# Optimization experiments

Measured on AMD Instinct MI355X. Metric: run time of the kernel, lower is better.

## Reference

```python
import jax, jax.numpy as jnp
import numpy as np

T, C, H, N = 1024, 2048, 32, 64
D_LORA, D_G = 64, 128

def _ln(x, w, b, eps=1e-5):
    m = x.mean(-1, keepdims=True)
    v = ((x - m) ** 2).mean(-1, keepdims=True)
    return (x - m) * jax.lax.rsqrt(v + eps) * w + b

def setup_inputs():
    key = jax.random.key(0)
    ks = iter(jax.random.split(key, 48))
    rn = lambda shape, s=1.0: jax.random.normal(next(ks), shape, dtype=jnp.float32) * s
    return {
        "x": rn((T, C)),
        "x_prev_att": rn((C,)),
        "vk_state": rn((H, N, N), 0.1),
        "x_prev_ffn": rn((C,)),
        "v_first": rn((T, C)),
        "ln1_w": jnp.ones((C,), jnp.float32), "ln1_b": jnp.zeros((C,), jnp.float32),
        "x_r": rn((C,), 0.1), "x_w": rn((C,), 0.1), "x_k": rn((C,), 0.1),
        "x_v": rn((C,), 0.1), "x_a": rn((C,), 0.1), "x_g": rn((C,), 0.1),
        "w0": rn((C,), 0.1), "w1": rn((C, D_LORA), 0.02), "w2": rn((D_LORA, C), 0.02),
        "a0": rn((C,), 0.1), "a1": rn((C, D_LORA), 0.02), "a2": rn((D_LORA, C), 0.02),
        "v0": rn((C,), 0.1), "v1": rn((C, D_LORA), 0.02), "v2": rn((D_LORA, C), 0.02),
        "g1": rn((C, D_G), 0.02), "g2": rn((D_G, C), 0.02),
        "k_k": rn((C,), 0.1), "k_a": rn((C,), 0.1), "r_k": rn((C,), 0.1),
        "R_": rn((C, C), 0.02), "K_": rn((C, C), 0.02),
        "V_": rn((C, C), 0.02), "O_": rn((C, C), 0.02),
        "lnx_w": jnp.ones((C,), jnp.float32), "lnx_b": jnp.zeros((C,), jnp.float32),
        "ln2_w": jnp.ones((C,), jnp.float32), "ln2_b": jnp.zeros((C,), jnp.float32),
        "ffn_x_k": rn((C,), 0.1),
        "ffn_K": rn((C, 4 * C), 0.02), "ffn_V": rn((4 * C, C), 0.02),
    }

def reference(x, x_prev_att, vk_state, x_prev_ffn, v_first, ln1_w, ln1_b,
              x_r, x_w, x_k, x_v, x_a, x_g, w0, w1, w2, a0, a1, a2,
              v0, v1, v2, g1, g2, k_k, k_a, r_k, R_, K_, V_, O_,
              lnx_w, lnx_b, ln2_w, ln2_b, ffn_x_k, ffn_K, ffn_V):
    # ---- TMix: RWKV-7 time mixing (layer_id = 1, so v_first blend is active) ----
    xln = _ln(x, ln1_w, ln1_b)                                  # [T, C]
    dx = jnp.concatenate([x_prev_att[None, :], xln[:-1]], axis=0) - xln  # token shift
    xr, xw, xk, xv, xa, xg = (xln + dx * m for m in (x_r, x_w, x_k, x_v, x_a, x_g))
    r = xr @ R_
    w = jnp.tanh(xw @ w1) @ w2
    k = xk @ K_
    v = xv @ V_
    a = jax.nn.sigmoid(a0 + (xa @ a1) @ a2)
    g = jax.nn.sigmoid(xg @ g1) @ g2
    kk = (k * k_k).reshape(T, H, N)
    kk = kk / jnp.maximum(jnp.linalg.norm(kk, axis=-1, keepdims=True), 1e-12)  # L2 normalize per head
    k = k * (1.0 + (a - 1.0) * k_a)
    v = v + (v_first - v) * jax.nn.sigmoid(v0 + (xv @ v1) @ v2)  # layer_id != 0 path
    w = jnp.exp(-0.606531 * jax.nn.sigmoid(w0 + w))               # per-channel decay in (0,1)
    rh, kh, vh = r.reshape(T, H, N), k.reshape(T, H, N), v.reshape(T, H, N)
    ah, wh = a.reshape(T, H, N), w.reshape(T, H, N)

    def step(state, inp):
        # state: [H, N, N]; generalized delta rule: state*w + state@(-kk)(kk*a)^T + v k^T
        w_t, kk_t, a_t, k_t, v_t, r_t = inp
        ab = jnp.einsum('hi,hj->hij', -kk_t, kk_t * a_t)
        vk = jnp.einsum('hi,hj->hij', v_t, k_t)
        state = state * w_t[:, None, :] + jnp.einsum('hij,hjk->hik', state, ab) + vk
        return state, jnp.einsum('hij,hj->hi', state, r_t)

    vk_state, outs = jax.lax.scan(step, vk_state, (wh, kk, ah, kh, vh, rh))  # outs: [T, H, N]
    # group norm over H groups, eps = 0.00064, affine per-channel
    m = outs.mean(-1, keepdims=True)
    var = ((outs - m) ** 2).mean(-1, keepdims=True)
    gn = ((outs - m) * jax.lax.rsqrt(var + 0.00064)).reshape(T, C) * lnx_w + lnx_b
    bonus = ((r * k * r_k).reshape(T, H, N).sum(-1, keepdims=True) * vh).reshape(T, C)
    x = x + ((gn + bonus) * g) @ O_
    # ---- CMix: gated squared-ReLU MLP ----
    xln2 = _ln(x, ln2_w, ln2_b)
    dx2 = jnp.concatenate([x_prev_ffn[None, :], xln2[:-1]], axis=0) - xln2
    kf = jax.nn.relu((xln2 + dx2 * ffn_x_k) @ ffn_K) ** 2
    x = x + kf @ ffn_V
    return x
```

## Files before the change

### kernel.cpp

```cpp
#include <hip/hip_runtime.h>
#include <hip/hip_bf16.h>


#define T_ 1024
#define C_ 2048
#define H_ 32
#define NH 64

typedef __attribute__((ext_vector_type(8))) short short8v;
typedef __attribute__((ext_vector_type(4))) float f32x4;

__device__ __forceinline__ float bf2f(unsigned short u) {
  union { float f; unsigned int i; } c; c.i = ((unsigned int)u) << 16; return c.f;
}
__device__ __forceinline__ unsigned short f2bf(float f) {
  union { float f; unsigned int i; } c; c.f = f;
  unsigned int x = c.i;
  return (unsigned short)((x + 0x7fffu + ((x >> 16) & 1u)) >> 16);
}
__device__ __forceinline__ float sigm(float x) { return 1.f / (1.f + __expf(-x)); }

__device__ __forceinline__ void load8bf(const unsigned short* p, float* o) {
  union { int4 v; unsigned short u[8]; } c;
  c.v = *(const int4*)p;
#pragma unroll
  for (int i = 0; i < 8; ++i) o[i] = bf2f(c.u[i]);
}
__device__ __forceinline__ void store8bf(unsigned short* p, const float* o) {
  union { int4 v; unsigned short u[8]; } c;
#pragma unroll
  for (int i = 0; i < 8; ++i) c.u[i] = f2bf(o[i]);
  *(int4*)p = c.v;
}
__device__ __forceinline__ void load8f(const float* p, float* o) {
  float4 a = ((const float4*)p)[0], b = ((const float4*)p)[1];
  o[0] = a.x; o[1] = a.y; o[2] = a.z; o[3] = a.w;
  o[4] = b.x; o[5] = b.y; o[6] = b.z; o[7] = b.w;
}
__device__ __forceinline__ void load4f(const float* p, float* o) {
  float4 a = *(const float4*)p;
  o[0] = a.x; o[1] = a.y; o[2] = a.z; o[3] = a.w;
}

#define GLD16(g, l)                                                        \
  __builtin_amdgcn_global_load_lds(                                        \
      (const __attribute__((address_space(1))) void*)(g),                  \
      (__attribute__((address_space(3))) void*)(l), 16, 0, 0)

__global__ __launch_bounds__(256) void lnmix6_kernel(
    const float* __restrict__ x, const float* __restrict__ xprev,
    const float* __restrict__ lw, const float* __restrict__ lb,
    const float* __restrict__ mr, const float* __restrict__ mw,
    const float* __restrict__ mk, const float* __restrict__ mv,
    const float* __restrict__ ma, const float* __restrict__ mg,
    unsigned short* xr, unsigned short* xw, unsigned short* xk,
    unsigned short* xv, unsigned short* xa, unsigned short* xg) {
  int t = blockIdx.x, tid = threadIdx.x, c = tid * 8;
  float cur[8], prv[8];
  load8f(x + (size_t)t * C_ + c, cur);
  if (t == 0) load8f(xprev + c, prv);
  else load8f(x + (size_t)(t - 1) * C_ + c, prv);
  float sc = 0.f, qc = 0.f, sp = 0.f, qp = 0.f;
#pragma unroll
  for (int i = 0; i < 8; ++i) {
    sc += cur[i]; qc += cur[i] * cur[i];
    sp += prv[i]; qp += prv[i] * prv[i];
  }
  for (int m = 1; m < 64; m <<= 1) {
    sc += __shfl_xor(sc, m); qc += __shfl_xor(qc, m);
    sp += __shfl_xor(sp, m); qp += __shfl_xor(qp, m);
  }
  __shared__ float r4[4][4];
  if ((tid & 63) == 0) {
    r4[tid >> 6][0] = sc; r4[tid >> 6][1] = qc;
    r4[tid >> 6][2] = sp; r4[tid >> 6][3] = qp;
  }
  __syncthreads();
  sc = r4[0][0] + r4[1][0] + r4[2][0] + r4[3][0];
  qc = r4[0][1] + r4[1][1] + r4[2][1] + r4[3][1];
  sp = r4[0][2] + r4[1][2] + r4[2][2] + r4[3][2];
  qp = r4[0][3] + r4[1][3] + r4[2][3] + r4[3][3];
  float mc = sc * (1.f / C_);
  float rc = rsqrtf(qc * (1.f / C_) - mc * mc + 1e-5f);
  float mp = sp * (1.f / C_);
  float rp = rsqrtf(qp * (1.f / C_) - mp * mp + 1e-5f);
  float cw[8], cb[8];
  load8f(lw + c, cw); load8f(lb + c, cb);
  float curn[8], prvn[8];
#pragma unroll
  for (int i = 0; i < 8; ++i) {
    curn[i] = (cur[i] - mc) * rc * cw[i] + cb[i];
    prvn[i] = (t == 0) ? prv[i] : (prv[i] - mp) * rp * cw[i] + cb[i];
  }
  float cf[8], o[8];
  const float* coefs[6] = {mr, mw, mk, mv, ma, mg};
  unsigned short* outs6[6] = {xr, xw, xk, xv, xa, xg};
#pragma unroll
  for (int a = 0; a < 6; ++a) {
    load8f(coefs[a] + c, cf);
#pragma unroll
    for (int i = 0; i < 8; ++i) o[i] = curn[i] + (prvn[i] - curn[i]) * cf[i];
    store8bf(outs6[a] + (size_t)t * C_ + c, o);
  }
}

__global__ __launch_bounds__(256) void lnmix1_kernel(
    const float* __restrict__ x, const float* __restrict__ xprev,
    const float* __restrict__ lw, const float* __restrict__ lb,
    const float* __restrict__ coef, unsigned short* __restrict__ out) {
  int t = blockIdx.x, tid = threadIdx.x, c = tid * 8;
  float cur[8], prv[8];
  load8f(x + (size_t)t * C_ + c, cur);
  if (t == 0) load8f(xprev + c, prv);
  else load8f(x + (size_t)(t - 1) * C_ + c, prv);
  float sc = 0.f, qc = 0.f, sp = 0.f, qp = 0.f;
#pragma unroll
  for (int i = 0; i < 8; ++i) {
    sc += cur[i]; qc += cur[i] * cur[i];
    sp += prv[i]; qp += prv[i] * prv[i];
  }
  for (int m = 1; m < 64; m <<= 1) {
    sc += __shfl_xor(sc, m); qc += __shfl_xor(qc, m);
    sp += __shfl_xor(sp, m); qp += __shfl_xor(qp, m);
  }
  __shared__ float r4[4][4];
  if ((tid & 63) == 0) {
    r4[tid >> 6][0] = sc; r4[tid >> 6][1] = qc;
    r4[tid >> 6][2] = sp; r4[tid >> 6][3] = qp;
  }
  __syncthreads();
  sc = r4[0][0] + r4[1][0] + r4[2][0] + r4[3][0];
  qc = r4[0][1] + r4[1][1] + r4[2][1] + r4[3][1];
  sp = r4[0][2] + r4[1][2] + r4[2][2] + r4[3][2];
  qp = r4[0][3] + r4[1][3] + r4[2][3] + r4[3][3];
  float mc = sc * (1.f / C_);
  float rc = rsqrtf(qc * (1.f / C_) - mc * mc + 1e-5f);
  float mp = sp * (1.f / C_);
  float rp = rsqrtf(qp * (1.f / C_) - mp * mp + 1e-5f);
  float cw[8], cb[8], cf[8], o[8];
  load8f(lw + c, cw); load8f(lb + c, cb); load8f(coef + c, cf);
#pragma unroll
  for (int i = 0; i < 8; ++i) {
    float cn = (cur[i] - mc) * rc * cw[i] + cb[i];
    float pn = (t == 0) ? prv[i] : (prv[i] - mp) * rp * cw[i] + cb[i];
    o[i] = cn + (pn - cn) * cf[i];
  }
  store8bf(out + (size_t)t * C_ + c, o);
}

__device__ __forceinline__ void transpose_tile(
    const float* __restrict__ in, unsigned short* __restrict__ out,
    int R, int Cc, int bx, int by, unsigned short (*tile)[80]) {
  int c0 = bx * 64, r0 = by * 64;
  int rr = threadIdx.x >> 4, cq = threadIdx.x & 15;
#pragma unroll
  for (int i = 0; i < 4; ++i) {
    int r = rr + i * 16;
    float4 v = *(const float4*)(in + (size_t)(r0 + r) * Cc + c0 + cq * 4);
    tile[cq * 4 + 0][r] = f2bf(v.x);
    tile[cq * 4 + 1][r] = f2bf(v.y);
    tile[cq * 4 + 2][r] = f2bf(v.z);
    tile[cq * 4 + 3][r] = f2bf(v.w);
  }
  __syncthreads();
  int cr = threadIdx.x >> 2, rg = threadIdx.x & 3;
  int4 w0 = *(const int4*)&tile[cr][rg * 16];
  int4 w1 = *(const int4*)&tile[cr][rg * 16 + 8];
  unsigned short* op = out + (size_t)(c0 + cr) * R + r0 + rg * 16;
  *(int4*)op = w0;
  *(int4*)(op + 8) = w1;
}

__global__ __launch_bounds__(256) void transpose_kernel(
    const float* in0, const float* in1, const float* in2,
    unsigned short* o0, unsigned short* o1, unsigned short* o2,
    int R, int Cc) {
  const float* in = blockIdx.z == 0 ? in0 : (blockIdx.z == 1 ? in1 : in2);
  unsigned short* out = blockIdx.z == 0 ? o0 : (blockIdx.z == 1 ? o1 : o2);
  __shared__ __align__(16) unsigned short tile[64][80];
  transpose_tile(in, out, R, Cc, blockIdx.x, blockIdx.y, tile);
}

template <int EPI>
__global__ __launch_bounds__(256) void gemm2_kernel(
    const unsigned short* A0, const unsigned short* A1, const unsigned short* A2,
    const unsigned short* B0, const unsigned short* B1, const unsigned short* B2,
    void* C0, void* C1, void* C2, const float* __restrict__ addsrc,
    int M, int K, int N) {
  int z = blockIdx.z;
  const unsigned short* A = z == 0 ? A0 : (z == 1 ? A1 : A2);
  const unsigned short* Bt = z == 0 ? B0 : (z == 1 ? B1 : B2);
  void* Cout = z == 0 ? C0 : (z == 1 ? C1 : C2);
  __shared__ __align__(16) unsigned short As[2][128 * 32];
  __shared__ __align__(16) unsigned short Bs[2][128 * 32];
  const int tid = threadIdx.x, lane = tid & 63, wid = tid >> 6;
  const int bm = blockIdx.y * 128, bn = blockIdx.x * 128;
  const int wr = wid >> 1, wc = wid & 1;
  const int mrow = lane & 15, krow = lane >> 4;
  auto stage = [&](int buf, int kt) {
#pragma unroll
    for (int q = 0; q < 2; ++q) {
      int s = q * 2048 + tid * 8;
      int m = s >> 5, k = s & 31;
      GLD16(A + (size_t)(bm + m) * K + kt + k, &As[buf][s]);
      GLD16(Bt + (size_t)(bn + m) * K + kt + k, &Bs[buf][s]);
    }
  };
  f32x4 acc[4][4] = {};
  stage(0, 0);
  __syncthreads();
  int buf = 0;
  for (int kt = 0; kt < K; kt += 32) {
    if (kt + 32 < K) stage(buf ^ 1, kt + 32);
    short8v af[4], bfrag[4];
#pragma unroll
    for (int i = 0; i < 4; ++i)
      af[i] = *(const short8v*)&As[buf][(wr * 64 + i * 16 + mrow) * 32 + krow * 8];
#pragma unroll
    for (int j = 0; j < 4; ++j)
      bfrag[j] = *(const short8v*)&Bs[buf][(wc * 64 + j * 16 + mrow) * 32 + krow * 8];
#pragma unroll
    for (int i = 0; i < 4; ++i)
#pragma unroll
      for (int j = 0; j < 4; ++j)
        acc[i][j] = __builtin_amdgcn_mfma_f32_16x16x32_bf16(af[i], bfrag[j], acc[i][j], 0, 0, 0);
    __syncthreads();
    buf ^= 1;
  }
#pragma unroll
  for (int i = 0; i < 4; ++i)
#pragma unroll
    for (int j = 0; j < 4; ++j)
#pragma unroll
      for (int e = 0; e < 4; ++e) {
        int grow = bm + wr * 64 + i * 16 + (lane >> 4) * 4 + e;
        int gcol = bn + wc * 64 + j * 16 + (lane & 15);
        size_t off = (size_t)grow * N + gcol;
        float v = acc[i][j][e];
        if constexpr (EPI == 0) ((float*)Cout)[off] = v;
        else if constexpr (EPI == 1) ((float*)Cout)[off] = addsrc[off] + v;
        else { float r = v > 0.f ? v : 0.f; ((unsigned short*)Cout)[off] = f2bf(r * r); }
      }
}

__global__ __launch_bounds__(256) void gemm2ks_kernel(
    const unsigned short* __restrict__ A, const unsigned short* __restrict__ Bt,
    unsigned short* __restrict__ P, int M, int KH, int Ktot, int N) {
  int kz = blockIdx.z;
  const size_t kbase = (size_t)kz * KH;
  __shared__ __align__(16) unsigned short As[2][128 * 32];
  __shared__ __align__(16) unsigned short Bs[2][128 * 32];
  const int tid = threadIdx.x, lane = tid & 63, wid = tid >> 6;
  const int bm = blockIdx.y * 128, bn = blockIdx.x * 128;
  const int wr = wid >> 1, wc = wid & 1;
  const int mrow = lane & 15, krow = lane >> 4;
  auto stage = [&](int buf, int kt) {
#pragma unroll
    for (int q = 0; q < 2; ++q) {
      int s = q * 2048 + tid * 8;
      int m = s >> 5, k = s & 31;
      GLD16(A + (size_t)(bm + m) * Ktot + kbase + kt + k, &As[buf][s]);
      GLD16(Bt + (size_t)(bn + m) * Ktot + kbase + kt + k, &Bs[buf][s]);
    }
  };
  f32x4 acc[4][4] = {};
  stage(0, 0);
  __syncthreads();
  int buf = 0;
  for (int kt = 0; kt < KH; kt += 32) {
    if (kt + 32 < KH) stage(buf ^ 1, kt + 32);
    short8v af[4], bfrag[4];
#pragma unroll
    for (int i = 0; i < 4; ++i)
      af[i] = *(const short8v*)&As[buf][(wr * 64 + i * 16 + mrow) * 32 + krow * 8];
#pragma unroll
    for (int j = 0; j < 4; ++j)
      bfrag[j] = *(const short8v*)&Bs[buf][(wc * 64 + j * 16 + mrow) * 32 + krow * 8];
#pragma unroll
    for (int i = 0; i < 4; ++i)
#pragma unroll
      for (int j = 0; j < 4; ++j)
        acc[i][j] = __builtin_amdgcn_mfma_f32_16x16x32_bf16(af[i], bfrag[j], acc[i][j], 0, 0, 0);
    __syncthreads();
    buf ^= 1;
  }
  unsigned short* Pz = P + (size_t)kz * M * N;
#pragma unroll
  for (int i = 0; i < 4; ++i)
#pragma unroll
    for (int j = 0; j < 4; ++j)
#pragma unroll
      for (int e = 0; e < 4; ++e) {
        int grow = bm + wr * 64 + i * 16 + (lane >> 4) * 4 + e;
        int gcol = bn + wc * 64 + j * 16 + (lane & 15);
        Pz[(size_t)grow * N + gcol] = f2bf(acc[i][j][e]);
      }
}

__global__ __launch_bounds__(256) void gemm2ks3_kernel(
    const unsigned short* A0, const unsigned short* A1, const unsigned short* A2,
    const unsigned short* B0, const unsigned short* B1, const unsigned short* B2,
    unsigned short* __restrict__ P, int M, int KH, int Ktot, int N) {
  int z = blockIdx.z;
  int batch = z % 3, kz = z / 3;
  const unsigned short* A = batch == 0 ? A0 : (batch == 1 ? A1 : A2);
  const unsigned short* Bt = batch == 0 ? B0 : (batch == 1 ? B1 : B2);
  const size_t kbase = (size_t)kz * KH;
  __shared__ __align__(16) unsigned short As[2][128 * 32];
  __shared__ __align__(16) unsigned short Bs[2][128 * 32];
  const int tid = threadIdx.x, lane = tid & 63, wid = tid >> 6;
  const int bm = blockIdx.y * 128, bn = blockIdx.x * 128;
  const int wr = wid >> 1, wc = wid & 1;
  const int mrow = lane & 15, krow = lane >> 4;
  auto stage = [&](int buf, int kt) {
#pragma unroll
    for (int q = 0; q < 2; ++q) {
      int s = q * 2048 + tid * 8;
      int m = s >> 5, k = s & 31;
      GLD16(A + (size_t)(bm + m) * Ktot + kbase + kt + k, &As[buf][s]);
      GLD16(Bt + (size_t)(bn + m) * Ktot + kbase + kt + k, &Bs[buf][s]);
    }
  };
  f32x4 acc[4][4] = {};
  stage(0, 0);
  __syncthreads();
  int buf = 0;
  for (int kt = 0; kt < KH; kt += 32) {
    if (kt + 32 < KH) stage(buf ^ 1, kt + 32);
    short8v af[4], bfrag[4];
#pragma unroll
    for (int i = 0; i < 4; ++i)
      af[i] = *(const short8v*)&As[buf][(wr * 64 + i * 16 + mrow) * 32 + krow * 8];
#pragma unroll
    for (int j = 0; j < 4; ++j)
      bfrag[j] = *(const short8v*)&Bs[buf][(wc * 64 + j * 16 + mrow) * 32 + krow * 8];
#pragma unroll
    for (int i = 0; i < 4; ++i)
#pragma unroll
      for (int j = 0; j < 4; ++j)
        acc[i][j] = __builtin_amdgcn_mfma_f32_16x16x32_bf16(af[i], bfrag[j], acc[i][j], 0, 0, 0);
    __syncthreads();
    buf ^= 1;
  }
  unsigned short* Pz = P + (size_t)z * M * N;
#pragma unroll
  for (int i = 0; i < 4; ++i)
#pragma unroll
    for (int j = 0; j < 4; ++j)
#pragma unroll
      for (int e = 0; e < 4; ++e) {
        int grow = bm + wr * 64 + i * 16 + (lane >> 4) * 4 + e;
        int gcol = bn + wc * 64 + j * 16 + (lane & 15);
        Pz[(size_t)grow * N + gcol] = f2bf(acc[i][j][e]);
      }
}

__global__ __launch_bounds__(256) void add5_kernel(
    const float* __restrict__ a, const unsigned short* __restrict__ p,
    float* __restrict__ o) {
  size_t i = ((size_t)blockIdx.x * 256 + threadIdx.x) * 8;
  const size_t TC = (size_t)T_ * C_;
  float va[8], v0[8], v1[8], v2[8], v3[8], r[8];
  load8f(a + i, va);
  load8bf(p + i, v0);
  load8bf(p + i + TC, v1);
  load8bf(p + i + 2 * TC, v2);
  load8bf(p + i + 3 * TC, v3);
#pragma unroll
  for (int k = 0; k < 8; ++k) r[k] = va[k] + v0[k] + v1[k] + v2[k] + v3[k];
  *(float4*)(o + i) = make_float4(r[0], r[1], r[2], r[3]);
  *(float4*)(o + i + 4) = make_float4(r[4], r[5], r[6], r[7]);
}

__global__ __launch_bounds__(256) void add5tr_kernel(
    const float* __restrict__ a, const unsigned short* __restrict__ p,
    float* __restrict__ o, const float* __restrict__ fK,
    unsigned short* __restrict__ fKt) {
  int bid = blockIdx.x;
  if (bid < 1024) {
    size_t i = ((size_t)bid * 256 + threadIdx.x) * 8;
    const size_t TC = (size_t)T_ * C_;
    float va[8], v0[8], v1[8], v2[8], v3[8], r[8];
    load8f(a + i, va);
    load8bf(p + i, v0);
    load8bf(p + i + TC, v1);
    load8bf(p + i + 2 * TC, v2);
    load8bf(p + i + 3 * TC, v3);
#pragma unroll
    for (int k = 0; k < 8; ++k) r[k] = va[k] + v0[k] + v1[k] + v2[k] + v3[k];
    *(float4*)(o + i) = make_float4(r[0], r[1], r[2], r[3]);
    *(float4*)(o + i + 4) = make_float4(r[4], r[5], r[6], r[7]);
    return;
  }
  __shared__ __align__(16) unsigned short tile[64][80];
  int idx = bid - 1024;
  transpose_tile(fK, fKt, C_, 4 * C_, idx & 127, idx >> 7, tile);
}

__global__ __launch_bounds__(256) void gemm_ks3_kernel(
    const unsigned short* A0, const unsigned short* A1, const unsigned short* A2,
    const unsigned short* B0, const unsigned short* B1, const unsigned short* B2,
    float* P0, float* P1, float* P2, int K, int N) {
  int mz = blockIdx.z >> 3, kz = blockIdx.z & 7;
  const unsigned short* A = mz == 0 ? A0 : (mz == 1 ? A1 : A2);
  const unsigned short* Bt = mz == 0 ? B0 : (mz == 1 ? B1 : B2);
  float* partial = mz == 0 ? P0 : (mz == 1 ? P1 : P2);
  __shared__ __align__(16) unsigned short As[2][128 * 32];
  __shared__ __align__(16) unsigned short Bs[2][64 * 32];
  const int tid = threadIdx.x, lane = tid & 63, wid = tid >> 6;
  const int bn = blockIdx.x * 64, bm = blockIdx.y * 128;
  const int wr = wid >> 1, wc = wid & 1;
  const int mrow = lane & 15, krow = lane >> 4;
  auto stage = [&](int buf, int kt) {
#pragma unroll
    for (int q = 0; q < 2; ++q) {
      int s = q * 2048 + tid * 8;
      int m = s >> 5, k = s & 31;
      GLD16(A + (size_t)(bm + m) * K + kt + k, &As[buf][s]);
    }
    {
      int s = tid * 8;
      int n = s >> 5, k = s & 31;
      GLD16(Bt + (size_t)(bn + n) * K + kt + k, &Bs[buf][s]);
    }
  };
  f32x4 acc[4][2] = {};
  int k0 = kz * 256;
  stage(0, k0);
  __syncthreads();
  int buf = 0;
  for (int kt = k0; kt < k0 + 256; kt += 32) {
    if (kt + 32 < k0 + 256) stage(buf ^ 1, kt + 32);
    short8v af[4], bfrag[2];
#pragma unroll
    for (int i = 0; i < 4; ++i)
      af[i] = *(const short8v*)&As[buf][(wr * 64 + i * 16 + mrow) * 32 + krow * 8];
#pragma unroll
    for (int j = 0; j < 2; ++j)
      bfrag[j] = *(const short8v*)&Bs[buf][(wc * 32 + j * 16 + mrow) * 32 + krow * 8];
#pragma unroll
    for (int i = 0; i < 4; ++i)
#pragma unroll
      for (int j = 0; j < 2; ++j)
        acc[i][j] = __builtin_amdgcn_mfma_f32_16x16x32_bf16(af[i], bfrag[j], acc[i][j], 0, 0, 0);
    __syncthreads();
    buf ^= 1;
  }
#pragma unroll
  for (int i = 0; i < 4; ++i)
#pragma unroll
    for (int j = 0; j < 2; ++j)
#pragma unroll
      for (int e = 0; e < 4; ++e) {
        int row = bm + wr * 64 + i * 16 + (lane >> 4) * 4 + e;
        int col = bn + wc * 32 + j * 16 + (lane & 15);
        partial[((size_t)kz * 1024 + row) * N + col] = acc[i][j][e];
      }
}

__global__ __launch_bounds__(256) void gemm_ks_kernel(
    const unsigned short* __restrict__ A, const unsigned short* __restrict__ Bt,
    float* __restrict__ partial, int K, int N) {
  __shared__ __align__(16) unsigned short As[2][128 * 32];
  __shared__ __align__(16) unsigned short Bs[2][64 * 32];
  const int tid = threadIdx.x, lane = tid & 63, wid = tid >> 6;
  const int bn = blockIdx.x * 64, bm = blockIdx.y * 128, kz = blockIdx.z;
  const int wr = wid >> 1, wc = wid & 1;
  const int mrow = lane & 15, krow = lane >> 4;
  auto stage = [&](int buf, int kt) {
#pragma unroll
    for (int q = 0; q < 2; ++q) {
      int s = q * 2048 + tid * 8;
      int m = s >> 5, k = s & 31;
      GLD16(A + (size_t)(bm + m) * K + kt + k, &As[buf][s]);
    }
    {
      int s = tid * 8;
      int n = s >> 5, k = s & 31;
      GLD16(Bt + (size_t)(bn + n) * K + kt + k, &Bs[buf][s]);
    }
  };
  f32x4 acc[4][2] = {};
  int k0 = kz * 256;
  stage(0, k0);
  __syncthreads();
  int buf = 0;
  for (int kt = k0; kt < k0 + 256; kt += 32) {
    if (kt + 32 < k0 + 256) stage(buf ^ 1, kt + 32);
    short8v af[4], bfrag[2];
#pragma unroll
    for (int i = 0; i < 4; ++i)
      af[i] = *(const short8v*)&As[buf][(wr * 64 + i * 16 + mrow) * 32 + krow * 8];
#pragma unroll
    for (int j = 0; j < 2; ++j)
      bfrag[j] = *(const short8v*)&Bs[buf][(wc * 32 + j * 16 + mrow) * 32 + krow * 8];
#pragma unroll
    for (int i = 0; i < 4; ++i)
#pragma unroll
      for (int j = 0; j < 2; ++j)
        acc[i][j] = __builtin_amdgcn_mfma_f32_16x16x32_bf16(af[i], bfrag[j], acc[i][j], 0, 0, 0);
    __syncthreads();
    buf ^= 1;
  }
#pragma unroll
  for (int i = 0; i < 4; ++i)
#pragma unroll
    for (int j = 0; j < 2; ++j)
#pragma unroll
      for (int e = 0; e < 4; ++e) {
        int row = bm + wr * 64 + i * 16 + (lane >> 4) * 4 + e;
        int col = bn + wc * 32 + j * 16 + (lane & 15);
        partial[((size_t)kz * 1024 + row) * N + col] = acc[i][j][e];
      }
}

__global__ __launch_bounds__(128) void lora_combine_kernel(
    const float* __restrict__ pw, const float* __restrict__ pa,
    const float* __restrict__ pv, const float* __restrict__ pg,
    unsigned short* __restrict__ hw, unsigned short* __restrict__ ha,
    unsigned short* __restrict__ hv, unsigned short* __restrict__ hg) {
  int t = blockIdx.x, which = blockIdx.y, tid = threadIdx.x;
  int Nl = (which == 3) ? 128 : 64;
  if (tid >= Nl) return;
  const float* p = which == 0 ? pw : which == 1 ? pa : which == 2 ? pv : pg;
  float s = 0.f;
#pragma unroll
  for (int kz = 0; kz < 8; ++kz) s += p[((size_t)kz * 1024 + t) * Nl + tid];
  float r = which == 0 ? tanhf(s) : (which == 3 ? sigm(s) : s);
  unsigned short* o = which == 0 ? hw : which == 1 ? ha : which == 2 ? hv : hg;
  o[t * Nl + tid] = f2bf(r);
}

__global__ __launch_bounds__(256) void post_kernel(
    const unsigned short* __restrict__ qRKV, const float* __restrict__ wpre,
    const float* __restrict__ apre, const float* __restrict__ vpre,
    const float* __restrict__ vfirst, const float* __restrict__ w0,
    const float* __restrict__ a0, const float* __restrict__ v0_,
    const float* __restrict__ k_k, const float* __restrict__ k_a,
    float* __restrict__ scanin) {
  int t = blockIdx.x, tid = threadIdx.x;
  int c = tid * 8, h = tid >> 3, j = c & 63;
  size_t o = (size_t)t * C_ + c;
  const size_t TC = (size_t)T_ * C_;
  float rv[8], kv[8], vv[8], t0[8], wv[8], av[8], vp[8], vf[8];
  load8bf(qRKV + o, rv);          load8bf(qRKV + 3 * TC + o, t0);
#pragma unroll
  for (int i = 0; i < 8; ++i) rv[i] += t0[i];
  load8bf(qRKV + TC + o, kv);     load8bf(qRKV + 4 * TC + o, t0);
#pragma unroll
  for (int i = 0; i < 8; ++i) kv[i] += t0[i];
  load8bf(qRKV + 2 * TC + o, vv); load8bf(qRKV + 5 * TC + o, t0);
#pragma unroll
  for (int i = 0; i < 8; ++i) vv[i] += t0[i];
  load8f(wpre + o, wv); load8f(apre + o, av); load8f(vpre + o, vp);
  load8f(vfirst + o, vf);
  float ckk[8], cka[8], cw0[8], ca0[8], cv0[8];
  load8f(k_k + c, ckk); load8f(k_a + c, cka); load8f(w0 + c, cw0);
  load8f(a0 + c, ca0); load8f(v0_ + c, cv0);
  float kk[8]; float ss = 0.f;
#pragma unroll
  for (int i = 0; i < 8; ++i) { kk[i] = kv[i] * ckk[i]; ss += kk[i] * kk[i]; }
  ss += __shfl_xor(ss, 1); ss += __shfl_xor(ss, 2); ss += __shfl_xor(ss, 4);
  float rdn = 1.f / fmaxf(sqrtf(ss), 1e-12f);
  float sw[8], skn[8], scc[8], sk2[8], sv[8];
#pragma unroll
  for (int i = 0; i < 8; ++i) {
// ... 153 lines not shown
  const float* x       = (const float*)d_in[0];
  const float* xprev_a = (const float*)d_in[1];
  const float* vk0     = (const float*)d_in[2];
  const float* xprev_f = (const float*)d_in[3];
  const float* vfirst  = (const float*)d_in[4];
  const float* ln1w = (const float*)d_in[5];
  const float* ln1b = (const float*)d_in[6];
  const float* m_r = (const float*)d_in[7];
  const float* m_w = (const float*)d_in[8];
  const float* m_k = (const float*)d_in[9];
  const float* m_v = (const float*)d_in[10];
  const float* m_a = (const float*)d_in[11];
  const float* m_g = (const float*)d_in[12];
  const float* w0 = (const float*)d_in[13];
  const float* w1 = (const float*)d_in[14];
  const float* w2 = (const float*)d_in[15];
  const float* a0 = (const float*)d_in[16];
  const float* a1 = (const float*)d_in[17];
  const float* a2 = (const float*)d_in[18];
  const float* v0 = (const float*)d_in[19];
  const float* v1 = (const float*)d_in[20];
  const float* v2 = (const float*)d_in[21];
  const float* g1 = (const float*)d_in[22];
  const float* g2 = (const float*)d_in[23];
  const float* k_k = (const float*)d_in[24];
  const float* k_a = (const float*)d_in[25];
  const float* r_k = (const float*)d_in[26];
  const float* R_ = (const float*)d_in[27];
  const float* K_ = (const float*)d_in[28];
  const float* V_ = (const float*)d_in[29];
  const float* O_ = (const float*)d_in[30];
  const float* lnxw = (const float*)d_in[31];
  const float* lnxb = (const float*)d_in[32];
  const float* ln2w = (const float*)d_in[33];
  const float* ln2b = (const float*)d_in[34];
  const float* fxk = (const float*)d_in[35];
  const float* fK = (const float*)d_in[36];
  const float* fV = (const float*)d_in[37];
  float* out = (float*)d_out;

  char* ws = (char*)d_ws;
  const size_t MB = 1ull << 20;
  unsigned short* attin = (unsigned short*)(ws + 0 * MB);
  unsigned short* xr    = (unsigned short*)(ws + 4 * MB);
  unsigned short* xw    = (unsigned short*)(ws + 8 * MB);
  unsigned short* xk    = (unsigned short*)(ws + 12 * MB);
  unsigned short* xv    = (unsigned short*)(ws + 16 * MB);
  unsigned short* xa    = (unsigned short*)(ws + 20 * MB);
  unsigned short* xg    = (unsigned short*)(ws + 24 * MB);
  float* wpre  = (float*)(ws + 4 * MB);
  float* apre  = (float*)(ws + 12 * MB);
  float* vpre  = (float*)(ws + 20 * MB);
  unsigned short* fVt = (unsigned short*)(ws + 4 * MB);
  unsigned short* xkf = (unsigned short*)(ws + 36 * MB);
  unsigned short* qRKV = (unsigned short*)(ws + 28 * MB);
  float* outsb = (float*)(ws + 52 * MB);
  unsigned short* Ot = (unsigned short*)(ws + 60 * MB);
  float* x_att = (float*)(ws + 60 * MB);
  float* g_buf = (float*)(ws + 76 * MB);
  float* scanin = (float*)(ws + 84 * MB);
  unsigned short* Rt  = (unsigned short*)(ws + 84 * MB);
  unsigned short* Kt  = (unsigned short*)(ws + 92 * MB);
  unsigned short* Vt  = (unsigned short*)(ws + 100 * MB);
  unsigned short* qO  = (unsigned short*)(ws + 84 * MB);
  unsigned short* hffn = (unsigned short*)(ws + 84 * MB);
  unsigned short* fKt  = (unsigned short*)(ws + 100 * MB);
  unsigned short* pF   = (unsigned short*)(ws + 100 * MB);
  unsigned short* w1t = (unsigned short*)(ws + 0);
  unsigned short* a1t = (unsigned short*)(ws + 262144);
  unsigned short* v1t = (unsigned short*)(ws + 524288);
  unsigned short* g1t = (unsigned short*)(ws + 786432);
  unsigned short* w2t = (unsigned short*)(ws + 0);
  unsigned short* a2t = (unsigned short*)(ws + 262144);
  unsigned short* v2t = (unsigned short*)(ws + 524288);
  unsigned short* g2t = (unsigned short*)(ws + 786432);
  unsigned short* hwb = (unsigned short*)(ws + 1376256);
  unsigned short* hab = (unsigned short*)(ws + 1507328);
  unsigned short* hvb = (unsigned short*)(ws + 1638400);
  unsigned short* hgb = (unsigned short*)(ws + 1769472);
  float* pw = (float*)(ws + 2 * MB);
  float* pa = (float*)(ws + 4 * MB);
  float* pv = (float*)(ws + 6 * MB);
  float* pg = (float*)(ws + 8 * MB);

  lnmix6_kernel<<<T_, 256, 0, stream>>>(x, xprev_a, ln1w, ln1b,
                                        m_r, m_w, m_k, m_v, m_a, m_g,
                                        xr, xw, xk, xv, xa, xg);
  transpose_kernel<<<dim3(32, 32, 3), 256, 0, stream>>>(R_, K_, V_, Rt, Kt, Vt, C_, C_);
  gemm2ks3_kernel<<<dim3(16, 8, 6), 256, 0, stream>>>(xr, xk, xv, Rt, Kt, Vt,
                                                      qRKV, T_, 1024, C_, C_);
  transpose_kernel<<<dim3(1, 32, 3), 256, 0, stream>>>(w1, a1, v1, w1t, a1t, v1t, C_, 64);
  transpose_kernel<<<dim3(2, 32, 1), 256, 0, stream>>>(g1, g1, g1, g1t, g1t, g1t, C_, 128);
  gemm_ks3_kernel<<<dim3(1, 8, 24), 256, 0, stream>>>(xw, xa, xv, w1t, a1t, v1t,
                                                      pw, pa, pv, C_, 64);
  gemm_ks_kernel<<<dim3(2, 8, 8), 256, 0, stream>>>(xg, g1t, pg, C_, 128);
  lora_combine_kernel<<<dim3(T_, 4), 128, 0, stream>>>(pw, pa, pv, pg, hwb, hab, hvb, hgb);
  transpose_kernel<<<dim3(32, 1, 3), 256, 0, stream>>>(w2, a2, v2, w2t, a2t, v2t, 64, C_);
  transpose_kernel<<<dim3(32, 2, 1), 256, 0, stream>>>(g2, g2, g2, g2t, g2t, g2t, 128, C_);
  gemm2_kernel<0><<<dim3(16, 8, 3), 256, 0, stream>>>(hwb, hab, hvb, w2t, a2t, v2t,
                                                      wpre, apre, vpre, nullptr, T_, 64, C_);
  gemm2_kernel<0><<<dim3(16, 8, 1), 256, 0, stream>>>(hgb, hgb, hgb, g2t, g2t, g2t,
                                                      g_buf, g_buf, g_buf, nullptr, T_, 128, C_);
  post_kernel<<<T_, 256, 0, stream>>>(qRKV, wpre, apre, vpre, vfirst,
                                      w0, a0, v0, k_k, k_a, scanin);
  scanfuse_kernel<<<5632, 256, 0, stream>>>(scanin, vk0, outsb, O_, Ot, fV, fVt);
  gnb_kernel<<<T_, 256, 0, stream>>>(outsb, scanin, g_buf, r_k, lnxw, lnxb, attin);
  gemm2ks_kernel<<<dim3(16, 8, 4), 256, 0, stream>>>(attin, Ot, qO, T_, 512, C_, C_);
  add5tr_kernel<<<5120, 256, 0, stream>>>(x, qO, x_att, fK, fKt);
  lnmix1_kernel<<<T_, 256, 0, stream>>>(x_att, xprev_f, ln2w, ln2b, fxk, xkf);
  gemm2_kernel<2><<<dim3(64, 8, 1), 256, 0, stream>>>(xkf, xkf, xkf, fKt, fKt, fKt,
                                                      hffn, hffn, hffn, nullptr, T_, C_, 4 * C_);
  gemm2ks_kernel<<<dim3(16, 8, 4), 256, 0, stream>>>(hffn, fVt, pF, T_, 2048, 4 * C_, C_);
  add5_kernel<<<1024, 256, 0, stream>>>(x_att, pF, out);
}
```

Measured before the change: 451.2 us.

## Merge LN-mix with all weight transposes and batch the front GEMMs into one launch

Folds the six weight transposes into the first layer-norm/mix kernel as extra blocks. It also merges the R/K/V split-K GEMM and the LoRA down-projection GEMMs into a single heterogeneous launch, and the four LoRA up-projection GEMMs into one launch. This cuts around nine kernel launches and lets small LoRA GEMMs fill the GPU alongside the large ones, at the cost of relocating workspace buffers so the merged stages do not alias. Blocks in the fused kernels take divergent paths and share one LDS allocation sized for the largest role.

```diff
diff --git a/kernel.cpp b/kernel.cpp
--- a/kernel.cpp
+++ b/kernel.cpp
@@ -47,15 +47,78 @@
       (const __attribute__((address_space(1))) void*)(g),                  \
       (__attribute__((address_space(3))) void*)(l), 16, 0, 0)
 
-__global__ __launch_bounds__(256) void lnmix6_kernel(
+__device__ __forceinline__ void transpose_tile(
+    const float* __restrict__ in, unsigned short* __restrict__ out,
+    int R, int Cc, int bx, int by, unsigned short (*tile)[80]) {
+  int c0 = bx * 64, r0 = by * 64;
+  int rr = threadIdx.x >> 4, cq = threadIdx.x & 15;
+#pragma unroll
+  for (int i = 0; i < 4; ++i) {
+    int r = rr + i * 16;
+    float4 v = *(const float4*)(in + (size_t)(r0 + r) * Cc + c0 + cq * 4);
+    tile[cq * 4 + 0][r] = f2bf(v.x);
+    tile[cq * 4 + 1][r] = f2bf(v.y);
+    tile[cq * 4 + 2][r] = f2bf(v.z);
+    tile[cq * 4 + 3][r] = f2bf(v.w);
+  }
+  __syncthreads();
+  int cr = threadIdx.x >> 2, rg = threadIdx.x & 3;
+  int4 w0 = *(const int4*)&tile[cr][rg * 16];
+  int4 w1 = *(const int4*)&tile[cr][rg * 16 + 8];
+  unsigned short* op = out + (size_t)(c0 + cr) * R + r0 + rg * 16;
+  *(int4*)op = w0;
+  *(int4*)(op + 8) = w1;
+}
+
+__global__ __launch_bounds__(256) void lnmix6tr_kernel(
     const float* __restrict__ x, const float* __restrict__ xprev,
     const float* __restrict__ lw, const float* __restrict__ lb,
     const float* __restrict__ mr, const float* __restrict__ mw,
     const float* __restrict__ mk, const float* __restrict__ mv,
     const float* __restrict__ ma, const float* __restrict__ mg,
     unsigned short* xr, unsigned short* xw, unsigned short* xk,
-    unsigned short* xv, unsigned short* xa, unsigned short* xg) {
-  int t = blockIdx.x, tid = threadIdx.x, c = tid * 8;
+    unsigned short* xv, unsigned short* xa, unsigned short* xg,
+    const float* R_, const float* K_, const float* V_,
+    unsigned short* Rt, unsigned short* Kt, unsigned short* Vt,
+    const float* w1, const float* a1, const float* v1,
+    unsigned short* w1t, unsigned short* a1t, unsigned short* v1t,
+    const float* g1, unsigned short* g1t,
+    const float* w2, const float* a2, const float* v2,
+    unsigned short* w2t, unsigned short* a2t, unsigned short* v2t,
+    const float* g2, unsigned short* g2t) {
+  __shared__ __align__(16) unsigned short tile[64][80];
+  __shared__ float r4[4][4];
+  int bid = blockIdx.x;
+  if (bid >= 1024) {
+    int idx = bid - 1024;
+    if (idx < 3072) {
+      const float* in = idx < 1024 ? R_ : (idx < 2048 ? K_ : V_);
+      unsigned short* out = idx < 1024 ? Rt : (idx < 2048 ? Kt : Vt);
+      int r = idx & 1023;
+      transpose_tile(in, out, C_, C_, r & 31, r >> 5, tile);
+      return;
+    }
+    idx -= 3072;
+    if (idx < 96) {
+      const float* in = idx < 32 ? w1 : (idx < 64 ? a1 : v1);
+      unsigned short* out = idx < 32 ? w1t : (idx < 64 ? a1t : v1t);
+      transpose_tile(in, out, C_, 64, 0, idx & 31, tile);
+      return;
+    }
+    idx -= 96;
+    if (idx < 64) { transpose_tile(g1, g1t, C_, 128, idx & 1, idx >> 1, tile); return; }
+    idx -= 64;
+    if (idx < 96) {
+      const float* in = idx < 32 ? w2 : (idx < 64 ? a2 : v2);
+      unsigned short* out = idx < 32 ? w2t : (idx < 64 ? a2t : v2t);
+      transpose_tile(in, out, 64, C_, idx & 31, 0, tile);
+      return;
+    }
+    idx -= 96;
+    transpose_tile(g2, g2t, 128, C_, idx & 31, idx >> 5, tile);
+    return;
+  }
+  int t = bid, tid = threadIdx.x, c = tid * 8;
   float cur[8], prv[8];
   load8f(x + (size_t)t * C_ + c, cur);
   if (t == 0) load8f(xprev + c, prv);
@@ -70,7 +133,6 @@
     sc += __shfl_xor(sc, m); qc += __shfl_xor(qc, m);
     sp += __shfl_xor(sp, m); qp += __shfl_xor(qp, m);
   }
-  __shared__ float r4[4][4];
   if ((tid & 63) == 0) {
     r4[tid >> 6][0] = sc; r4[tid >> 6][1] = qc;
     r4[tid >> 6][2] = sp; r4[tid >> 6][3] = qp;
@@ -146,39 +208,6 @@
     o[i] = cn + (pn - cn) * cf[i];
   }
   store8bf(out + (size_t)t * C_ + c, o);
-}
-
-__device__ __forceinline__ void transpose_tile(
-    const float* __restrict__ in, unsigned short* __restrict__ out,
-    int R, int Cc, int bx, int by, unsigned short (*tile)[80]) {
-  int c0 = bx * 64, r0 = by * 64;
-  int rr = threadIdx.x >> 4, cq = threadIdx.x & 15;
-#pragma unroll
-  for (int i = 0; i < 4; ++i) {
-    int r = rr + i * 16;
-    float4 v = *(const float4*)(in + (size_t)(r0 + r) * Cc + c0 + cq * 4);
-    tile[cq * 4 + 0][r] = f2bf(v.x);
-    tile[cq * 4 + 1][r] = f2bf(v.y);
-    tile[cq * 4 + 2][r] = f2bf(v.z);
-    tile[cq * 4 + 3][r] = f2bf(v.w);
-  }
-  __syncthreads();
-  int cr = threadIdx.x >> 2, rg = threadIdx.x & 3;
-  int4 w0 = *(const int4*)&tile[cr][rg * 16];
-  int4 w1 = *(const int4*)&tile[cr][rg * 16 + 8];
-  unsigned short* op = out + (size_t)(c0 + cr) * R + r0 + rg * 16;
-  *(int4*)op = w0;
-  *(int4*)(op + 8) = w1;
-}
-
-__global__ __launch_bounds__(256) void transpose_kernel(
-    const float* in0, const float* in1, const float* in2,
-    unsigned short* o0, unsigned short* o1, unsigned short* o2,
-    int R, int Cc) {
-  const float* in = blockIdx.z == 0 ? in0 : (blockIdx.z == 1 ? in1 : in2);
-  unsigned short* out = blockIdx.z == 0 ? o0 : (blockIdx.z == 1 ? o1 : o2);
-  __shared__ __align__(16) unsigned short tile[64][80];
-  transpose_tile(in, out, R, Cc, blockIdx.x, blockIdx.y, tile);
 }
 
 template <int EPI>
@@ -243,6 +272,66 @@
       }
 }
 
+__global__ __launch_bounds__(256) void gemm2up_kernel(
+    const unsigned short* hwb, const unsigned short* hab,
+    const unsigned short* hvb, const unsigned short* hgb,
+    const unsigned short* w2t, const unsigned short* a2t,
+    const unsigned short* v2t, const unsigned short* g2t,
+    float* wpre, float* apre, float* vpre, float* g_buf) {
+  int z = blockIdx.z;
+  const unsigned short* A = z == 0 ? hwb : (z == 1 ? hab : (z == 2 ? hvb : hgb));
+  const unsigned short* Bt = z == 0 ? w2t : (z == 1 ? a2t : (z == 2 ? v2t : g2t));
+  float* Cout = z == 0 ? wpre : (z == 1 ? apre : (z == 2 ? vpre : g_buf));
+  const int K = (z == 3) ? 128 : 64;
+  const int N = C_;
+  __shared__ __align__(16) unsigned short As[2][128 * 32];
+  __shared__ __align__(16) unsigned short Bs[2][128 * 32];
+  const int tid = threadIdx.x, lane = tid & 63, wid = tid >> 6;
+  const int bm = blockIdx.y * 128, bn = blockIdx.x * 128;
+  const int wr = wid >> 1, wc = wid & 1;
+  const int mrow = lane & 15, krow = lane >> 4;
+  auto stage = [&](int buf, int kt) {
+#pragma unroll
+    for (int q = 0; q < 2; ++q) {
+      int s = q * 2048 + tid * 8;
+      int m = s >> 5, k = s & 31;
+      GLD16(A + (size_t)(bm + m) * K + kt + k, &As[buf][s]);
+      GLD16(Bt + (size_t)(bn + m) * K + kt + k, &Bs[buf][s]);
+    }
+  };
+  f32x4 acc[4][4] = {};
+  stage(0, 0);
+  __syncthreads();
+  int buf = 0;
+  for (int kt = 0; kt < K; kt += 32) {
+    if (kt + 32 < K) stage(buf ^ 1, kt + 32);
+    short8v af[4], bfrag[4];
+#pragma unroll
+    for (int i = 0; i < 4; ++i)
+      af[i] = *(const short8v*)&As[buf][(wr * 64 + i * 16 + mrow) * 32 + krow * 8];
+#pragma unroll
+    for (int j = 0; j < 4; ++j)
+      bfrag[j] = *(const short8v*)&Bs[buf][(wc * 64 + j * 16 + mrow) * 32 + krow * 8];
+#pragma unroll
+    for (int i = 0; i < 4; ++i)
+#pragma unroll
+      for (int j = 0; j < 4; ++j)
+        acc[i][j] = __builtin_amdgcn_mfma_f32_16x16x32_bf16(af[i], bfrag[j], acc[i][j], 0, 0, 0);
+    __syncthreads();
+    buf ^= 1;
+  }
+#pragma unroll
+  for (int i = 0; i < 4; ++i)
+#pragma unroll
+    for (int j = 0; j < 4; ++j)
+#pragma unroll
+      for (int e = 0; e < 4; ++e) {
+        int grow = bm + wr * 64 + i * 16 + (lane >> 4) * 4 + e;
+        int gcol = bn + wc * 64 + j * 16 + (lane & 15);
+        Cout[(size_t)grow * N + gcol] = acc[i][j][e];
+      }
+}
+
 __global__ __launch_bounds__(256) void gemm2ks_kernel(
     const unsigned short* __restrict__ A, const unsigned short* __restrict__ Bt,
     unsigned short* __restrict__ P, int M, int KH, int Ktot, int N) {
@@ -297,61 +386,136 @@
       }
 }
 
-__global__ __launch_bounds__(256) void gemm2ks3_kernel(
-    const unsigned short* A0, const unsigned short* A1, const unsigned short* A2,
-    const unsigned short* B0, const unsigned short* B1, const unsigned short* B2,
-    unsigned short* __restrict__ P, int M, int KH, int Ktot, int N) {
-  int z = blockIdx.z;
-  int batch = z % 3, kz = z / 3;
-  const unsigned short* A = batch == 0 ? A0 : (batch == 1 ? A1 : A2);
-  const unsigned short* Bt = batch == 0 ? B0 : (batch == 1 ? B1 : B2);
-  const size_t kbase = (size_t)kz * KH;
-  __shared__ __align__(16) unsigned short As[2][128 * 32];
-  __shared__ __align__(16) unsigned short Bs[2][128 * 32];
+__global__ __launch_bounds__(256) void bigemm_kernel(
+    const unsigned short* xr, const unsigned short* xk, const unsigned short* xv,
+    const unsigned short* Rt, const unsigned short* Kt, const unsigned short* Vt,
+    unsigned short* __restrict__ qRKV,
+    const unsigned short* xw, const unsigned short* xa, const unsigned short* xg,
+    const unsigned short* w1t, const unsigned short* a1t, const unsigned short* v1t,
+    const unsigned short* g1t,
+    float* pw, float* pa, float* pv, float* pg) {
+  __shared__ __align__(16) unsigned short smem[16384];
+  const int bid = blockIdx.x;
   const int tid = threadIdx.x, lane = tid & 63, wid = tid >> 6;
-  const int bm = blockIdx.y * 128, bn = blockIdx.x * 128;
   const int wr = wid >> 1, wc = wid & 1;
   const int mrow = lane & 15, krow = lane >> 4;
+  unsigned short* As0 = smem;
+  if (bid < 768) {
+    int bz = bid >> 7, rem = bid & 127;
+    int bx = rem & 15, by = rem >> 4;
+    int batch = bz % 3, kz = bz / 3;
+    const unsigned short* A = batch == 0 ? xr : (batch == 1 ? xk : xv);
+    const unsigned short* Bt = batch == 0 ? Rt : (batch == 1 ? Kt : Vt);
+    unsigned short* Bs0 = smem + 8192;
+    const size_t kbase = (size_t)kz * 1024;
+    const int bm = by * 128, bn = bx * 128;
+    auto stage = [&](int buf, int kt) {
+#pragma unroll
+      for (int q = 0; q < 2; ++q) {
+        int s = q * 2048 + tid * 8;
+        int m = s >> 5, k = s & 31;
+        GLD16(A + (size_t)(bm + m) * C_ + kbase + kt + k, &As0[buf * 4096 + s]);
+        GLD16(Bt + (size_t)(bn + m) * C_ + kbase + kt + k, &Bs0[buf * 4096 + s]);
+      }
+    };
+    f32x4 acc[4][4] = {};
+    stage(0, 0);
+    __syncthreads();
+    int buf = 0;
+    for (int kt = 0; kt < 1024; kt += 32) {
+      if (kt + 32 < 1024) stage(buf ^ 1, kt + 32);
+      short8v af[4], bfrag[4];
+#pragma unroll
+      for (int i = 0; i < 4; ++i)
+        af[i] = *(const short8v*)&As0[buf * 4096 + (wr * 64 + i * 16 + mrow) * 32 + krow * 8];
+#pragma unroll
+      for (int j = 0; j < 4; ++j)
+        bfrag[j] = *(const short8v*)&Bs0[buf * 4096 + (wc * 64 + j * 16 + mrow) * 32 + krow * 8];
+#pragma unroll
+      for (int i = 0; i < 4; ++i)
+#pragma unroll
+        for (int j = 0; j < 4; ++j)
+          acc[i][j] = __builtin_amdgcn_mfma_f32_16x16x32_bf16(af[i], bfrag[j], acc[i][j], 0, 0, 0);
+      __syncthreads();
+      buf ^= 1;
+    }
+    unsigned short* Pz = qRKV + (size_t)bz * T_ * C_;
+#pragma unroll
+    for (int i = 0; i < 4; ++i)
+#pragma unroll
+      for (int j = 0; j < 4; ++j)
+#pragma unroll
+        for (int e = 0; e < 4; ++e) {
+          int grow = bm + wr * 64 + i * 16 + (lane >> 4) * 4 + e;
+          int gcol = bn + wc * 64 + j * 16 + (lane & 15);
+          Pz[(size_t)grow * C_ + gcol] = f2bf(acc[i][j][e]);
+        }
+    return;
+  }
+  const unsigned short* A;
+  const unsigned short* Bt;
+  float* partial;
+  int N, bn, bm, kz;
+  if (bid < 960) {
+    int idx = bid - 768;
+    int by = idx & 7, kzz = idx >> 3;
+    int mz = kzz >> 3; kz = kzz & 7;
+    A = mz == 0 ? xw : (mz == 1 ? xa : xv);
+    Bt = mz == 0 ? w1t : (mz == 1 ? a1t : v1t);
+    partial = mz == 0 ? pw : (mz == 1 ? pa : pv);
+    N = 64; bn = 0; bm = by * 128;
+  } else {
+    int idx = bid - 960;
+    kz = idx >> 4;
+    int rem = idx & 15;
+    A = xg; Bt = g1t; partial = pg;
+    N = 128; bn = (rem & 1) * 64; bm = (rem >> 1) * 128;
+  }
+  unsigned short* Bs0 = smem + 8192;
   auto stage = [&](int buf, int kt) {
 #pragma unroll
     for (int q = 0; q < 2; ++q) {
       int s = q * 2048 + tid * 8;
       int m = s >> 5, k = s & 31;
-      GLD16(A + (size_t)(bm + m) * Ktot + kbase + kt + k, &As[buf][s]);
-      GLD16(Bt + (size_t)(bn + m) * Ktot + kbase + kt + k, &Bs[buf][s]);
+      GLD16(A + (size_t)(bm + m) * C_ + kt + k, &As0[buf * 4096 + s]);
+    }
+    {
+      int s = tid * 8;
+      int n = s >> 5, k = s & 31;
+      GLD16(Bt + (size_t)(bn + n) * C_ + kt + k, &Bs0[buf * 2048 + s]);
     }
   };
-  f32x4 acc[4][4] = {};
-  stage(0, 0);
+  f32x4 acc[4][2] = {};
+  int k0 = kz * 256;
+  stage(0, k0);
   __syncthreads();
   int buf = 0;
-  for (int kt = 0; kt < KH; kt += 32) {
-    if (kt + 32 < KH) stage(buf ^ 1, kt + 32);
-    short8v af[4], bfrag[4];
+  for (int kt = k0; kt < k0 + 256; kt += 32) {
+    if (kt + 32 < k0 + 256) stage(buf ^ 1, kt + 32);
+    short8v af[4], bfrag[2];
 #pragma unroll
     for (int i = 0; i < 4; ++i)
-      af[i] = *(const short8v*)&As[buf][(wr * 64 + i * 16 + mrow) * 32 + krow * 8];
-#pragma unroll
-    for (int j = 0; j < 4; ++j)
-      bfrag[j] = *(const short8v*)&Bs[buf][(wc * 64 + j * 16 + mrow) * 32 + krow * 8];
+      af[i] = *(const short8v*)&As0[buf * 4096 + (wr * 64 + i * 16 + mrow) * 32 + krow * 8];
+#pragma unroll
+    for (int j = 0; j < 2; ++j)
+      bfrag[j] = *(const short8v*)&Bs0[buf * 2048 + (wc * 32 + j * 16 + mrow) * 32 + krow * 8];
 #pragma unroll
     for (int i = 0; i < 4; ++i)
 #pragma unroll
-      for (int j = 0; j < 4; ++j)
+      for (int j = 0; j < 2; ++j)
         acc[i][j] = __builtin_amdgcn_mfma_f32_16x16x32_bf16(af[i], bfrag[j], acc[i][j], 0, 0, 0);
     __syncthreads();
     buf ^= 1;
   }
-  unsigned short* Pz = P + (size_t)z * M * N;
 #pragma unroll
   for (int i = 0; i < 4; ++i)
 #pragma unroll
-    for (int j = 0; j < 4; ++j)
+    for (int j = 0; j < 2; ++j)
 #pragma unroll
       for (int e = 0; e < 4; ++e) {
-        int grow = bm + wr * 64 + i * 16 + (lane >> 4) * 4 + e;
-        int gcol = bn + wc * 64 + j * 16 + (lane & 15);
-        Pz[(size_t)grow * N + gcol] = f2bf(acc[i][j][e]);
+        int row = bm + wr * 64 + i * 16 + (lane >> 4) * 4 + e;
+        int col = bn + wc * 32 + j * 16 + (lane & 15);
+        partial[((size_t)kz * 1024 + row) * N + col] = acc[i][j][e];
       }
 }
 
@@ -395,123 +559,6 @@
   __shared__ __align__(16) unsigned short tile[64][80];
   int idx = bid - 1024;
   transpose_tile(fK, fKt, C_, 4 * C_, idx & 127, idx >> 7, tile);
-}
-
-__global__ __launch_bounds__(256) void gemm_ks3_kernel(
-    const unsigned short* A0, const unsigned short* A1, const unsigned short* A2,
-    const unsigned short* B0, const unsigned short* B1, const unsigned short* B2,
-    float* P0, float* P1, float* P2, int K, int N) {
-  int mz = blockIdx.z >> 3, kz = blockIdx.z & 7;
-  const unsigned short* A = mz == 0 ? A0 : (mz == 1 ? A1 : A2);
-  const unsigned short* Bt = mz == 0 ? B0 : (mz == 1 ? B1 : B2);
-  float* partial = mz == 0 ? P0 : (mz == 1 ? P1 : P2);
-  __shared__ __align__(16) unsigned short As[2][128 * 32];
-  __shared__ __align__(16) unsigned short Bs[2][64 * 32];
-  const int tid = threadIdx.x, lane = tid & 63, wid = tid >> 6;
-  const int bn = blockIdx.x * 64, bm = blockIdx.y * 128;
-  const int wr = wid >> 1, wc = wid & 1;
-  const int mrow = lane & 15, krow = lane >> 4;
-  auto stage = [&](int buf, int kt) {
-#pragma unroll
-    for (int q = 0; q < 2; ++q) {
-      int s = q * 2048 + tid * 8;
-      int m = s >> 5, k = s & 31;
-      GLD16(A + (size_t)(bm + m) * K + kt + k, &As[buf][s]);
-    }
-    {
-      int s = tid * 8;
-      int n = s >> 5, k = s & 31;
-      GLD16(Bt + (size_t)(bn + n) * K + kt + k, &Bs[buf][s]);
-    }
-  };
-  f32x4 acc[4][2] = {};
-  int k0 = kz * 256;
-  stage(0, k0);
-  __syncthreads();
-  int buf = 0;
-  for (int kt = k0; kt < k0 + 256; kt += 32) {
-    if (kt + 32 < k0 + 256) stage(buf ^ 1, kt + 32);
-    short8v af[4], bfrag[2];
-#pragma unroll
-    for (int i = 0; i < 4; ++i)
-      af[i] = *(const short8v*)&As[buf][(wr * 64 + i * 16 + mrow) * 32 + krow * 8];
-#pragma unroll
-    for (int j = 0; j < 2; ++j)
-      bfrag[j] = *(const short8v*)&Bs[buf][(wc * 32 + j * 16 + mrow) * 32 + krow * 8];
-#pragma unroll
-    for (int i = 0; i < 4; ++i)
-#pragma unroll
-      for (int j = 0; j < 2; ++j)
-        acc[i][j] = __builtin_amdgcn_mfma_f32_16x16x32_bf16(af[i], bfrag[j], acc[i][j], 0, 0, 0);
-    __syncthreads();
-    buf ^= 1;
-  }
-#pragma unroll
-  for (int i = 0; i < 4; ++i)
-#pragma unroll
-    for (int j = 0; j < 2; ++j)
-#pragma unroll
-      for (int e = 0; e < 4; ++e) {
-        int row = bm + wr * 64 + i * 16 + (lane >> 4) * 4 + e;
-        int col = bn + wc * 32 + j * 16 + (lane & 15);
-        partial[((size_t)kz * 1024 + row) * N + col] = acc[i][j][e];
-      }
-}
-
-__global__ __launch_bounds__(256) void gemm_ks_kernel(
-    const unsigned short* __restrict__ A, const unsigned short* __restrict__ Bt,
-    float* __restrict__ partial, int K, int N) {
-  __shared__ __align__(16) unsigned short As[2][128 * 32];
-  __shared__ __align__(16) unsigned short Bs[2][64 * 32];
-  const int tid = threadIdx.x, lane = tid & 63, wid = tid >> 6;
-  const int bn = blockIdx.x * 64, bm = blockIdx.y * 128, kz = blockIdx.z;
-  const int wr = wid >> 1, wc = wid & 1;
-  const int mrow = lane & 15, krow = lane >> 4;
-  auto stage = [&](int buf, int kt) {
-#pragma unroll
-    for (int q = 0; q < 2; ++q) {
-      int s = q * 2048 + tid * 8;
-      int m = s >> 5, k = s & 31;
-      GLD16(A + (size_t)(bm + m) * K + kt + k, &As[buf][s]);
-    }
-    {
-      int s = tid * 8;
-      int n = s >> 5, k = s & 31;
-      GLD16(Bt + (size_t)(bn + n) * K + kt + k, &Bs[buf][s]);
-    }
-  };
-  f32x4 acc[4][2] = {};
-  int k0 = kz * 256;
-  stage(0, k0);
-  __syncthreads();
-  int buf = 0;
-  for (int kt = k0; kt < k0 + 256; kt += 32) {
-    if (kt + 32 < k0 + 256) stage(buf ^ 1, kt + 32);
-    short8v af[4], bfrag[2];
-#pragma unroll
-    for (int i = 0; i < 4; ++i)
-      af[i] = *(const short8v*)&As[buf][(wr * 64 + i * 16 + mrow) * 32 + krow * 8];
-#pragma unroll
-    for (int j = 0; j < 2; ++j)
-      bfrag[j] = *(const short8v*)&Bs[buf][(wc * 32 + j * 16 + mrow) * 32 + krow * 8];
-#pragma unroll
-    for (int i = 0; i < 4; ++i)
-#pragma unroll
-      for (int j = 0; j < 2; ++j)
-        acc[i][j] = __builtin_amdgcn_mfma_f32_16x16x32_bf16(af[i], bfrag[j], acc[i][j], 0, 0, 0);
-    __syncthreads();
-    buf ^= 1;
-  }
-#pragma unroll
-  for (int i = 0; i < 4; ++i)
-#pragma unroll
-    for (int j = 0; j < 2; ++j)
-#pragma unroll
-      for (int e = 0; e < 4; ++e) {
-        int row = bm + wr * 64 + i * 16 + (lane >> 4) * 4 + e;
-        int col = bn + wc * 32 + j * 16 + (lane & 15);
-        partial[((size_t)kz * 1024 + row) * N + col] = acc[i][j][e];
-      }
 }
 
 __global__ __launch_bounds__(128) void lora_combine_kernel(
@@ -771,11 +818,15 @@
   float* apre  = (float*)(ws + 12 * MB);
   float* vpre  = (float*)(ws + 20 * MB);
   unsigned short* fVt = (unsigned short*)(ws + 4 * MB);
-  unsigned short* xkf = (unsigned short*)(ws + 36 * MB);
   unsigned short* qRKV = (unsigned short*)(ws + 28 * MB);
   float* outsb = (float*)(ws + 52 * MB);
   unsigned short* Ot = (unsigned short*)(ws + 60 * MB);
   float* x_att = (float*)(ws + 60 * MB);
+  unsigned short* xkf = (unsigned short*)(ws + 68 * MB);
+  unsigned short* w2t = (unsigned short*)(ws + 72 * MB);
+  unsigned short* a2t = (unsigned short*)(ws + 72 * MB + 262144);
+  unsigned short* v2t = (unsigned short*)(ws + 72 * MB + 524288);
+  unsigned short* g2t = (unsigned short*)(ws + 72 * MB + 786432);
   float* g_buf = (float*)(ws + 76 * MB);
   float* scanin = (float*)(ws + 84 * MB);
   unsigned short* Rt  = (unsigned short*)(ws + 84 * MB);
@@ -785,41 +836,32 @@
   unsigned short* hffn = (unsigned short*)(ws + 84 * MB);
   unsigned short* fKt  = (unsigned short*)(ws + 100 * MB);
   unsigned short* pF   = (unsigned short*)(ws + 100 * MB);
+  float* pw = (float*)(ws + 108 * MB);
+  float* pa = (float*)(ws + 110 * MB);
+  float* pv = (float*)(ws + 112 * MB);
+  float* pg = (float*)(ws + 114 * MB);
   unsigned short* w1t = (unsigned short*)(ws + 0);
   unsigned short* a1t = (unsigned short*)(ws + 262144);
   unsigned short* v1t = (unsigned short*)(ws + 524288);
   unsigned short* g1t = (unsigned short*)(ws + 786432);
-  unsigned short* w2t = (unsigned short*)(ws + 0);
-  unsigned short* a2t = (unsigned short*)(ws + 262144);
-  unsigned short* v2t = (unsigned short*)(ws + 524288);
-  unsigned short* g2t = (unsigned short*)(ws + 786432);
   unsigned short* hwb = (unsigned short*)(ws + 1376256);
   unsigned short* hab = (unsigned short*)(ws + 1507328);
   unsigned short* hvb = (unsigned short*)(ws + 1638400);
   unsigned short* hgb = (unsigned short*)(ws + 1769472);
-  float* pw = (float*)(ws + 2 * MB);
-  float* pa = (float*)(ws + 4 * MB);
-  float* pv = (float*)(ws + 6 * MB);
-  float* pg = (float*)(ws + 8 * MB);
-
-  lnmix6_kernel<<<T_, 256, 0, stream>>>(x, xprev_a, ln1w, ln1b,
-                                        m_r, m_w, m_k, m_v, m_a, m_g,
-                                        xr, xw, xk, xv, xa, xg);
-  transpose_kernel<<<dim3(32, 32, 3), 256, 0, stream>>>(R_, K_, V_, Rt, Kt, Vt, C_, C_);
-  gemm2ks3_kernel<<<dim3(16, 8, 6), 256, 0, stream>>>(xr, xk, xv, Rt, Kt, Vt,
-                                                      qRKV, T_, 1024, C_, C_);
-  transpose_kernel<<<dim3(1, 32, 3), 256, 0, stream>>>(w1, a1, v1, w1t, a1t, v1t, C_, 64);
-  transpose_kernel<<<dim3(2, 32, 1), 256, 0, stream>>>(g1, g1, g1, g1t, g1t, g1t, C_, 128);
-  gemm_ks3_kernel<<<dim3(1, 8, 24), 256, 0, stream>>>(xw, xa, xv, w1t, a1t, v1t,
-                                                      pw, pa, pv, C_, 64);
-  gemm_ks_kernel<<<dim3(2, 8, 8), 256, 0, stream>>>(xg, g1t, pg, C_, 128);
+
+  lnmix6tr_kernel<<<4416, 256, 0, stream>>>(
+      x, xprev_a, ln1w, ln1b, m_r, m_w, m_k, m_v, m_a, m_g,
+      xr, xw, xk, xv, xa, xg,
+      R_, K_, V_, Rt, Kt, Vt,
+      w1, a1, v1, w1t, a1t, v1t, g1, g1t,
+      w2, a2, v2, w2t, a2t, v2t, g2, g2t);
+  bigemm_kernel<<<1088, 256, 0, stream>>>(xr, xk, xv, Rt, Kt, Vt, qRKV,
+                                          xw, xa, xg, w1t, a1t, v1t, g1t,
+                                          pw, pa, pv, pg);
   lora_combine_kernel<<<dim3(T_, 4), 128, 0, stream>>>(pw, pa, pv, pg, hwb, hab, hvb, hgb);
-  transpose_kernel<<<dim3(32, 1, 3), 256, 0, stream>>>(w2, a2, v2, w2t, a2t, v2t, 64, C_);
-  transpose_kernel<<<dim3(32, 2, 1), 256, 0, stream>>>(g2, g2, g2, g2t, g2t, g2t, 128, C_);
-  gemm2_kernel<0><<<dim3(16, 8, 3), 256, 0, stream>>>(hwb, hab, hvb, w2t, a2t, v2t,
-                                                      wpre, apre, vpre, nullptr, T_, 64, C_);
-  gemm2_kernel<0><<<dim3(16, 8, 1), 256, 0, stream>>>(hgb, hgb, hgb, g2t, g2t, g2t,
-                                                      g_buf, g_buf, g_buf, nullptr, T_, 128, C_);
+  gemm2up_kernel<<<dim3(16, 8, 4), 256, 0, stream>>>(hwb, hab, hvb, hgb,
+                                                     w2t, a2t, v2t, g2t,
+                                                     wpre, apre, vpre, g_buf);
   post_kernel<<<T_, 256, 0, stream>>>(qRKV, wpre, apre, vpre, vfirst,
                                       w0, a0, v0, k_k, k_a, scanin);
   scanfuse_kernel<<<5632, 256, 0, stream>>>(scanin, vk0, outsb, O_, Ot, fV, fVt);
```

New measurement: 429.0 us. 1.05x faster.
